# Performance work log

Hardware: AMD Instinct MI355X
Metric: run time of the kernel (lower is better)

## Reference

```python
import jax, jax.numpy as jnp
import numpy as np

B, D, C = 1024, 512, 100000
S, M = 64.0, 0.35
EPS = 1e-12  # torch F.normalize eps


def setup_inputs() -> dict:
    key = jax.random.key(0)
    k1, k2, k3 = jax.random.split(key, 3)
    inp = jax.random.normal(k1, (B, D), dtype=jnp.float32)
    label = jax.random.randint(k2, (B,), 0, C, dtype=jnp.int64)
    weight = jax.random.normal(k3, (C, D), dtype=jnp.float32) * (6.0 / (C + D)) ** 0.5
    return {"input": inp, "label": label, "weight": weight}


def _l2norm(x):
    n = jnp.linalg.norm(x, axis=-1, keepdims=True)
    return x / jnp.maximum(n, EPS)


def reference(input, label, weight):
    # cosine similarities: [B, C]
    cosine = _l2norm(input) @ _l2norm(weight).T
    # subtract margin only at the label position (no dense one-hot materialized)
    rows = jnp.arange(cosine.shape[0])
    logits = S * cosine.at[rows, label].add(-M)
    # cross-entropy (mean reduction)
    logz = jax.nn.logsumexp(logits, axis=-1)
    tgt = logits[rows, label]
    return jnp.mean(logz - tgt)
```

## Files before the change

kernel.cpp:

```cpp
#include <hip/hip_runtime.h>
#include <hip/hip_bf16.h>
#include <stdint.h>

#define NB 1024
#define ND 512
#define NC 100000
#define NCT 782
#define NCT2 391
#define SSCALE 64.0f
#define SMARG 22.4f

typedef __attribute__((ext_vector_type(8))) short bf16x8;
typedef __attribute__((ext_vector_type(4))) float f32x4;
typedef __attribute__((ext_vector_type(4))) int   i32x4;

__device__ __forceinline__ unsigned int f2bf(float f) {
    union { float f; unsigned int u; } c; c.f = f;
    return (c.u + 0x7fffu + ((c.u >> 16) & 1u)) >> 16;
}

__device__ __forceinline__ float wave_sum(float v) {
    #pragma unroll
    for (int m = 32; m > 0; m >>= 1) v += __shfl_xor(v, m);
    return v;
}

__device__ __forceinline__ float wave_max(float v) {
    #pragma unroll
    for (int m = 32; m > 0; m >>= 1) v = fmaxf(v, __shfl_xor(v, m));
    return v;
}

__device__ __forceinline__ void load_lds16(const void* g, void* l) {
    auto gp = reinterpret_cast<const __attribute__((address_space(1))) void*>(
        (uintptr_t)g);
    auto lp = reinterpret_cast<__attribute__((address_space(3))) void*>(
        (uint32_t)(uintptr_t)l);
    __builtin_amdgcn_global_load_lds(gp, lp, 16, 0, 0);
}

__global__ void norm_input_i8_k(const float* __restrict__ x,
                                unsigned char* __restrict__ xq,
                                float* __restrict__ isx) {
    int lane = threadIdx.x & 63;
    int row = blockIdx.x * 4 + (threadIdx.x >> 6);
    const float* xr = x + (size_t)row * ND + lane * 8;
    float4 v0 = ((const float4*)xr)[0];
    float4 v1 = ((const float4*)xr)[1];
    float ss = v0.x*v0.x + v0.y*v0.y + v0.z*v0.z + v0.w*v0.w
             + v1.x*v1.x + v1.y*v1.y + v1.z*v1.z + v1.w*v1.w;
    ss = wave_sum(ss);
    float inv = 1.0f / fmaxf(sqrtf(ss), 1e-12f);
    float f[8] = {v0.x*inv, v0.y*inv, v0.z*inv, v0.w*inv,
                  v1.x*inv, v1.y*inv, v1.z*inv, v1.w*inv};
    float ma = 0.0f;
    #pragma unroll
    for (int j = 0; j < 8; ++j) ma = fmaxf(ma, fabsf(f[j]));
    ma = wave_max(ma);
    ma = fmaxf(ma, 1e-12f);
    float s = 127.0f / ma;
    int q[8];
    #pragma unroll
    for (int j = 0; j < 8; ++j) q[j] = (int)rintf(f[j] * s);
    uint2 o;
    o.x = (q[0]&255) | ((q[1]&255)<<8) | ((q[2]&255)<<16) | ((unsigned)(q[3]&255)<<24);
    o.y = (q[4]&255) | ((q[5]&255)<<8) | ((q[6]&255)<<16) | ((unsigned)(q[7]&255)<<24);
    *(uint2*)(xq + (size_t)row * ND + lane * 8) = o;
    if (lane == 0) isx[row] = ma * (1.0f / 127.0f);
}

__global__ void conv_weight_i8_k(const float* __restrict__ w,
                                 unsigned char* __restrict__ wq,
                                 float* __restrict__ isw) {
    int lane = threadIdx.x & 63;
    int row = blockIdx.x * 4 + (threadIdx.x >> 6);
    const float* wr = w + (size_t)row * ND + lane * 8;
    float4 v0 = ((const float4*)wr)[0];
    float4 v1 = ((const float4*)wr)[1];
    float ss = v0.x*v0.x + v0.y*v0.y + v0.z*v0.z + v0.w*v0.w
             + v1.x*v1.x + v1.y*v1.y + v1.z*v1.z + v1.w*v1.w;
    ss = wave_sum(ss);
    float inv = 1.0f / fmaxf(sqrtf(ss), 1e-12f);
    float f[8] = {v0.x*inv, v0.y*inv, v0.z*inv, v0.w*inv,
                  v1.x*inv, v1.y*inv, v1.z*inv, v1.w*inv};
    float ma = 0.0f;
    #pragma unroll
    for (int j = 0; j < 8; ++j) ma = fmaxf(ma, fabsf(f[j]));
    ma = wave_max(ma);
    ma = fmaxf(ma, 1e-12f);
    float s = 127.0f / ma;
    int q[8];
    #pragma unroll
    for (int j = 0; j < 8; ++j) q[j] = (int)rintf(f[j] * s);
    uint2 o;
    o.x = (q[0]&255) | ((q[1]&255)<<8) | ((q[2]&255)<<16) | ((unsigned)(q[3]&255)<<24);
    o.y = (q[4]&255) | ((q[5]&255)<<8) | ((q[6]&255)<<16) | ((unsigned)(q[7]&255)<<24);
    *(uint2*)(wq + (size_t)row * ND + lane * 8) = o;
    if (lane == 0) isw[row] = ma * (1.0f / 127.0f);
}

__global__ __launch_bounds__(512, 2) void gemm_i8_k(
    const unsigned char* __restrict__ xq, const unsigned char* __restrict__ wq,
    const float* __restrict__ isx, const float* __restrict__ isw,
    const int* __restrict__ label,
    float* __restrict__ partial, float* __restrict__ tgt) {

    __shared__ __align__(16) char Tb[2][32768];
    __shared__ float rowsum[4][256];
    __shared__ int labs[256];
    __shared__ float isxs[256];
    __shared__ float isws[256];

    const int orig = blockIdx.x + (blockIdx.y << 2);
    const int xcd = orig & 7, idx = orig >> 3;
    const int wg = (xcd < 4 ? xcd * 196 : 784 + (xcd - 4) * 195) + idx;
    const int bx = wg & 3;
    const int by = wg >> 2;

    const int tid = threadIdx.x;
    const int lane = tid & 63;
    const int wid  = tid >> 6;
    const int brow0 = bx * 256;
    const int crow0 = by * 256;

    if (tid < 256) {
        labs[tid] = label[brow0 + tid];
        isxs[tid] = isx[brow0 + tid];
        int c = crow0 + tid;
        isws[tid] = (c < NC) ? isw[c] : 1.0f;
    }

    const unsigned char* gsrc[4];
    int ldst[4];
    #pragma unroll
    for (int i = 0; i < 4; ++i) {
        int cidx = wid * 256 + i * 64 + lane;
        int r = cidx >> 3, s = cidx & 7;
        int l = s ^ (r & 7);
        if (l < 4) {
            gsrc[i] = xq + (size_t)(brow0 + r) * ND + l * 16;
        } else {
            int wrow = crow0 + r;
            if (wrow >= NC) wrow = NC - 1;
            gsrc[i] = wq + (size_t)wrow * ND + (l - 4) * 16;
        }
        ldst[i] = cidx * 16;
    }

    const int wr = wid >> 2, wc = wid & 3;
    const int l15 = lane & 15, l4 = lane >> 4;

    i32x4 acc[8][4];
    #pragma unroll
    for (int i = 0; i < 8; ++i)
        #pragma unroll
        for (int j = 0; j < 4; ++j) acc[i][j] = (i32x4){0, 0, 0, 0};

    #pragma unroll
    for (int i = 0; i < 4; ++i) load_lds16(gsrc[i], &Tb[0][ldst[i]]);

    #pragma unroll
    for (int t = 0; t < 8; ++t) {
        __syncthreads();
        const char* cb = Tb[t & 1];
        i32x4 a0[4], a1[4], bfr[4];
        #pragma unroll
        for (int n = 0; n < 4; ++n) {
            int br = wc * 64 + n * 16 + l15;
            bfr[n] = *(const i32x4*)(cb + br * 128 + (((4 + l4) << 4) ^ ((br & 7) << 4)));
        }
        #pragma unroll
        for (int m = 0; m < 4; ++m) {
            int ar = wr * 128 + m * 16 + l15;
            a0[m] = *(const i32x4*)(cb + ar * 128 + ((l4 << 4) ^ ((ar & 7) << 4)));
        }
        if (t < 7) {
            char* nb = Tb[(t + 1) & 1];
            #pragma unroll
            for (int i = 0; i < 4; ++i)
                load_lds16(gsrc[i] + (t + 1) * 64, &nb[ldst[i]]);
        }
        #pragma unroll
        for (int m = 0; m < 4; ++m) {
            int ar = wr * 128 + (4 + m) * 16 + l15;
            a1[m] = *(const i32x4*)(cb + ar * 128 + ((l4 << 4) ^ ((ar & 7) << 4)));
        }
        __builtin_amdgcn_s_setprio(1);
        #pragma unroll
        for (int m = 0; m < 4; ++m)
            #pragma unroll
            for (int n = 0; n < 4; ++n)
                acc[m][n] = __builtin_amdgcn_mfma_i32_16x16x64_i8(
                    a0[m], bfr[n], acc[m][n], 0, 0, 0);
        __builtin_amdgcn_s_setprio(0);
        __builtin_amdgcn_s_setprio(1);
        #pragma unroll
        for (int m = 0; m < 4; ++m)
            #pragma unroll
            for (int n = 0; n < 4; ++n)
                acc[4 + m][n] = __builtin_amdgcn_mfma_i32_16x16x64_i8(
                    a1[m], bfr[n], acc[4 + m][n], 0, 0, 0);
        __builtin_amdgcn_s_setprio(0);
    }

    float rs[8][4];
    #pragma unroll
    for (int mi = 0; mi < 8; ++mi)
        #pragma unroll
        for (int r = 0; r < 4; ++r) rs[mi][r] = 0.0f;

    #pragma unroll
    for (int mi = 0; mi < 8; ++mi) {
        #pragma unroll
        for (int ni = 0; ni < 4; ++ni) {
            int ci = wc * 64 + ni * 16 + l15;
            int gc = crow0 + ci;
            float iw = isws[ci] * SSCALE;
            i32x4 av = acc[mi][ni];
            #pragma unroll
            for (int r = 0; r < 4; ++r) {
                int tr = wr * 128 + mi * 16 + l4 * 4 + r;
                float z = (float)av[r] * isxs[tr] * iw;
                if (gc == labs[tr]) {
                    z -= SMARG;
                    tgt[brow0 + tr] = z;
                }
                float e = (gc < NC) ? __expf(z - 64.0f) : 0.0f;
                rs[mi][r] += e;
            }
        }
    }
    #pragma unroll
    for (int mi = 0; mi < 8; ++mi)
        #pragma unroll
        for (int r = 0; r < 4; ++r) {
            float v = rs[mi][r];
            v += __shfl_xor(v, 1); v += __shfl_xor(v, 2);
            v += __shfl_xor(v, 4); v += __shfl_xor(v, 8);
            rs[mi][r] = v;
        }
    if (l15 == 0) {
        #pragma unroll
        for (int mi = 0; mi < 8; ++mi)
            #pragma unroll
            for (int r = 0; r < 4; ++r)
                rowsum[wc][wr * 128 + mi * 16 + l4 * 4 + r] = rs[mi][r];
    }
    __syncthreads();
    if (tid < 256)
        partial[(size_t)by * NB + brow0 + tid] =
            rowsum[0][tid] + rowsum[1][tid] + rowsum[2][tid] + rowsum[3][tid];
}

__global__ void norm_input_k(const float* __restrict__ x, unsigned short* __restrict__ xn) {
    int lane = threadIdx.x & 63;
    int row = blockIdx.x * 4 + (threadIdx.x >> 6);
    const float* xr = x + row * ND + lane * 8;
    float4 v0 = ((const float4*)xr)[0];
    float4 v1 = ((const float4*)xr)[1];
    float ss = v0.x*v0.x + v0.y*v0.y + v0.z*v0.z + v0.w*v0.w
             + v1.x*v1.x + v1.y*v1.y + v1.z*v1.z + v1.w*v1.w;
    ss = wave_sum(ss);
    float inv = 1.0f / fmaxf(sqrtf(ss), 1e-12f);
    int4 o;
    o.x = f2bf(v0.x*inv) | (f2bf(v0.y*inv) << 16);
    o.y = f2bf(v0.z*inv) | (f2bf(v0.w*inv) << 16);
    o.z = f2bf(v1.x*inv) | (f2bf(v1.y*inv) << 16);
    o.w = f2bf(v1.z*inv) | (f2bf(v1.w*inv) << 16);
    *(int4*)(xn + row * ND + lane * 8) = o;
}

__global__ void norm_weight_k(const float* __restrict__ w, float* __restrict__ invw) {
    int lane = threadIdx.x & 63;
    int row = blockIdx.x * 4 + (threadIdx.x >> 6);
    if (row >= NC) return;
    const float* wr = w + (size_t)row * ND + lane * 8;
    float4 v0 = ((const float4*)wr)[0];
    float4 v1 = ((const float4*)wr)[1];
    float ss = v0.x*v0.x + v0.y*v0.y + v0.z*v0.z + v0.w*v0.w
             + v1.x*v1.x + v1.y*v1.y + v1.z*v1.z + v1.w*v1.w;
    ss = wave_sum(ss);
    if (lane == 0) invw[row] = 1.0f / fmaxf(sqrtf(ss), 1e-12f);
}

__global__ __launch_bounds__(256) void gemm_fb_k(
    const unsigned short* __restrict__ xn, const float* __restrict__ w,
    const float* __restrict__ invw, const int* __restrict__ label,
    float* __restrict__ partial, float* __restrict__ tgt) {

    __shared__ __align__(16) char As[16384];
    __shared__ __align__(16) char Ws[16384];
    __shared__ float rowsum[2][128];
    __shared__ int labs[128];

    const int tid = threadIdx.x;
    const int brow0 = blockIdx.x * 128;
    const int crow0 = blockIdx.y * 128;

    if (tid < 128) labs[tid] = label[brow0 + tid];

    int arow[4], ac16[4];
    float wiv[4];
    bool  wval[4];
    #pragma unroll
    for (int i = 0; i < 4; ++i) {
        int idx = tid + i * 256;
        arow[i] = idx >> 3; ac16[i] = idx & 7;
        int grow = crow0 + (idx >> 3);
        wval[i] = grow < NC;
        wiv[i]  = wval[i] ? invw[grow] : 0.0f;
    }

    const int lane = tid & 63;
    const int wid  = tid >> 6;
    const int wr = wid >> 1, wc = wid & 1;
    const int l15 = lane & 15, l4 = lane >> 4;

    f32x4 acc[4][4];
    #pragma unroll
    for (int i = 0; i < 4; ++i)
        #pragma unroll
        for (int j = 0; j < 4; ++j) acc[i][j] = (f32x4){0.f, 0.f, 0.f, 0.f};

    for (int ks = 0; ks < 8; ++ks) {
        const int kbase = ks * 64;
        __syncthreads();
        #pragma unroll
        for (int i = 0; i < 4; ++i) {
            int row = arow[i], c16 = ac16[i];
            int4 v = *(const int4*)(xn + (brow0 + row) * ND + kbase + c16 * 8);
            *(int4*)(As + row * 128 + ((c16 * 16) ^ ((row & 7) << 4))) = v;
        }
        #pragma unroll
        for (int i = 0; i < 4; ++i) {
            int row = arow[i], c8 = ac16[i];
            float4 w0 = {0.f,0.f,0.f,0.f}, w1 = {0.f,0.f,0.f,0.f};
            if (wval[i]) {
                const float* wp = w + (size_t)(crow0 + row) * ND + kbase + c8 * 8;
                w0 = ((const float4*)wp)[0];
                w1 = ((const float4*)wp)[1];
            }
            float iv = wiv[i];
            int4 o;
            o.x = f2bf(w0.x*iv) | (f2bf(w0.y*iv) << 16);
            o.y = f2bf(w0.z*iv) | (f2bf(w0.w*iv) << 16);
            o.z = f2bf(w1.x*iv) | (f2bf(w1.y*iv) << 16);
            o.w = f2bf(w1.z*iv) | (f2bf(w1.w*iv) << 16);
            *(int4*)(Ws + row * 128 + ((c8 * 16) ^ ((row & 7) << 4))) = o;
        }
        __syncthreads();
        #pragma unroll
        for (int k32 = 0; k32 < 2; ++k32) {
            const int kb = k32 * 64 + l4 * 16;
            bf16x8 a[4], b[4];
            #pragma unroll
            for (int mi = 0; mi < 4; ++mi) {
                int ar = wr * 64 + mi * 16 + l15;
                a[mi] = *(const bf16x8*)(As + ar * 128 + (kb ^ ((ar & 7) << 4)));
            }
            #pragma unroll
            for (int ni = 0; ni < 4; ++ni) {
                int br = wc * 64 + ni * 16 + l15;
                b[ni] = *(const bf16x8*)(Ws + br * 128 + (kb ^ ((br & 7) << 4)));
            }
            #pragma unroll
            for (int mi = 0; mi < 4; ++mi)
                #pragma unroll
                for (int ni = 0; ni < 4; ++ni)
                    acc[mi][ni] = __builtin_amdgcn_mfma_f32_16x16x32_bf16(
                        a[mi], b[ni], acc[mi][ni], 0, 0, 0);
        }
    }

    float rs[4][4];
    #pragma unroll
    for (int mi = 0; mi < 4; ++mi)
        #pragma unroll
        for (int r = 0; r < 4; ++r) rs[mi][r] = 0.0f;

    #pragma unroll
    for (int mi = 0; mi < 4; ++mi) {
        #pragma unroll
        for (int ni = 0; ni < 4; ++ni) {
            int gc = crow0 + wc * 64 + ni * 16 + l15;
            f32x4 av = acc[mi][ni];
            #pragma unroll
            for (int r = 0; r < 4; ++r) {
                int tr = wr * 64 + mi * 16 + l4 * 4 + r;
                float z = SSCALE * av[r];
                if (gc == labs[tr]) {
                    z -= SMARG;
                    tgt[brow0 + tr] = z;
                }
                float e = (gc < NC) ? __expf(z - 64.0f) : 0.0f;
                rs[mi][r] += e;
            }
        }
    }
    #pragma unroll
    for (int mi = 0; mi < 4; ++mi)
        #pragma unroll
        for (int r = 0; r < 4; ++r) {
            float v = rs[mi][r];
            v += __shfl_xor(v, 1); v += __shfl_xor(v, 2);
            v += __shfl_xor(v, 4); v += __shfl_xor(v, 8);
            rs[mi][r] = v;
        }
    if (l15 == 0) {
        #pragma unroll
        for (int mi = 0; mi < 4; ++mi)
            #pragma unroll
            for (int r = 0; r < 4; ++r)
                rowsum[wc][wr * 64 + mi * 16 + l4 * 4 + r] = rs[mi][r];
    }
    __syncthreads();
    if (tid < 128)
        partial[(size_t)blockIdx.y * NB + brow0 + tid] = rowsum[0][tid] + rowsum[1][tid];
}

__global__ void row_lse_k(const float* __restrict__ partial, const float* __restrict__ tgt,
                          float* __restrict__ lossb, int nt) {
    int b = blockIdx.x;
    float s = 0.0f;
    for (int i = threadIdx.x; i < nt; i += 256)
        s += partial[(size_t)i * NB + b];
    s = wave_sum(s);
    __shared__ float wsum[4];
    if ((threadIdx.x & 63) == 0) wsum[threadIdx.x >> 6] = s;
    __syncthreads();
    if (threadIdx.x == 0)
        lossb[b] = 64.0f + logf(wsum[0] + wsum[1] + wsum[2] + wsum[3]) - tgt[b];
}

__global__ void mean_k(const float* __restrict__ lossb, float* __restrict__ out) {
    float s = 0.0f;
    for (int i = threadIdx.x; i < NB; i += 256) s += lossb[i];
    s = wave_sum(s);
    __shared__ float wsum[4];
    if ((threadIdx.x & 63) == 0) wsum[threadIdx.x >> 6] = s;
    __syncthreads();
    if (threadIdx.x == 0)
        out[0] = (wsum[0] + wsum[1] + wsum[2] + wsum[3]) * (1.0f / (float)NB);
}

extern "C" void kernel_launch(void* const* d_in, const int* in_sizes, int n_in,
                              void* d_out, int out_size, void* d_ws, size_t ws_size,
                              hipStream_t stream) {
    const float* x     = (const float*)d_in[0];
    const int*   label = (const int*)d_in[1];
    const float* w     = (const float*)d_in[2];
    float* out = (float*)d_out;
    char* ws = (char*)d_ws;

    const size_t WQ_B   = (size_t)NC * ND;
    const size_t ISW_B  = 400000;
    const size_t XQ_B   = (size_t)NB * ND;
    const size_t ISX_B  = 4096;
    const size_t PART2  = (size_t)NCT2 * NB * 4;
    const size_t FAST_REQ = WQ_B + ISW_B + XQ_B + ISX_B + PART2 + 8192;

    if (ws_size >= FAST_REQ) {
        unsigned char* wq      = (unsigned char*)(ws);
        float*         iswv    = (float*)(ws + WQ_B);
        unsigned char* xq      = (unsigned char*)(ws + WQ_B + ISW_B);
        float*         isxv    = (float*)(ws + WQ_B + ISW_B + XQ_B);
        float*         partial = (float*)(ws + WQ_B + ISW_B + XQ_B + ISX_B);
        float*         tgt     = (float*)(ws + WQ_B + ISW_B + XQ_B + ISX_B + PART2);
        float*         lossb   = (float*)(ws + WQ_B + ISW_B + XQ_B + ISX_B + PART2 + 4096);

        norm_input_i8_k <<<NB / 4, 256, 0, stream>>>(x, xq, isxv);
        conv_weight_i8_k<<<NC / 4, 256, 0, stream>>>(w, wq, iswv);
        dim3 grid(4, NCT2);
        gemm_i8_k<<<grid, 512, 0, stream>>>(xq, wq, isxv, iswv, label, partial, tgt);
        row_lse_k<<<NB, 256, 0, stream>>>(partial, tgt, lossb, NCT2);
        mean_k<<<1, 256, 0, stream>>>(lossb, out);
    } else {
        float*          invw    = (float*)(ws);
        unsigned short* xn      = (unsigned short*)(ws + 400384);
        float*          partial = (float*)(ws + 400384 + 1048576);
        float*          tgt     = (float*)(ws + 400384 + 1048576 + 3203072);
        float*          lossb   = (float*)(ws + 400384 + 1048576 + 3203072 + 4096);

        norm_input_k <<<NB / 4, 256, 0, stream>>>(x, xn);
        norm_weight_k<<<NC / 4, 256, 0, stream>>>(w, invw);
        dim3 grid(8, NCT);
        gemm_fb_k<<<grid, 256, 0, stream>>>(xn, w, invw, label, partial, tgt);
        row_lse_k<<<NB, 256, 0, stream>>>(partial, tgt, lossb, NCT);
        mean_k<<<1, 256, 0, stream>>>(lossb, out);
    }
}
```

Before: 164.0 us.

## Load weight fragments directly from global into registers, stage only input in LDS

The int8 GEMM now keeps only the input (A) tile in a smaller double-buffered LDS array, laid out so each lane reads its MFMA fragment contiguously. The weight (B) fragments are loaded straight from global memory into registers and prefetched one k-step ahead. This halves LDS traffic and LDS footprint, which may allow higher occupancy, and removes the swizzled LDS reads for B. In exchange each wave issues uncoalesced-ish 16-byte global loads for weights, depends on the register prefetch hiding latency, and uses more registers.

Result: slower. 207.5 us (+26.5%).

```diff
diff --git a/kernel.cpp b/kernel.cpp
--- a/kernel.cpp
+++ b/kernel.cpp
@@ -105,7 +105,7 @@
     const int* __restrict__ label,
     float* __restrict__ partial, float* __restrict__ tgt) {
 
-    __shared__ __align__(16) char Tb[2][32768];
+    __shared__ __align__(16) char Ab[2][16384];
     __shared__ float rowsum[4][256];
     __shared__ int labs[256];
     __shared__ float isxs[256];
@@ -130,77 +130,63 @@
         isws[tid] = (c < NC) ? isw[c] : 1.0f;
     }
 
-    const unsigned char* gsrc[4];
-    int ldst[4];
-    #pragma unroll
-    for (int i = 0; i < 4; ++i) {
-        int cidx = wid * 256 + i * 64 + lane;
-        int r = cidx >> 3, s = cidx & 7;
-        int l = s ^ (r & 7);
-        if (l < 4) {
-            gsrc[i] = xq + (size_t)(brow0 + r) * ND + l * 16;
-        } else {
-            int wrow = crow0 + r;
-            if (wrow >= NC) wrow = NC - 1;
-            gsrc[i] = wq + (size_t)wrow * ND + (l - 4) * 16;
-        }
-        ldst[i] = cidx * 16;
-    }
+    const int sr = tid & 255;
+    const int sc0 = tid >> 8;
+    const unsigned char* gA0 = xq + (size_t)(brow0 + sr) * ND + sc0 * 16;
+    const unsigned char* gA1 = gA0 + 32;
+    const int d0 = tid * 16;
+    const int d1 = d0 + 8192;
 
     const int wr = wid >> 2, wc = wid & 3;
     const int l15 = lane & 15, l4 = lane >> 4;
 
+    const unsigned char* gW[4];
+    #pragma unroll
+    for (int n = 0; n < 4; ++n) {
+        int br = crow0 + wc * 64 + n * 16 + l15;
+        if (br >= NC) br = NC - 1;
+        gW[n] = wq + (size_t)br * ND + l4 * 16;
+    }
+
     i32x4 acc[8][4];
     #pragma unroll
     for (int i = 0; i < 8; ++i)
         #pragma unroll
         for (int j = 0; j < 4; ++j) acc[i][j] = (i32x4){0, 0, 0, 0};
 
-    #pragma unroll
-    for (int i = 0; i < 4; ++i) load_lds16(gsrc[i], &Tb[0][ldst[i]]);
+    load_lds16(gA0, &Ab[0][d0]);
+    load_lds16(gA1, &Ab[0][d1]);
+    i32x4 wcur[4], wnxt[4];
+    #pragma unroll
+    for (int n = 0; n < 4; ++n) wcur[n] = *(const i32x4*)(gW[n]);
+    __syncthreads();
 
     #pragma unroll
     for (int t = 0; t < 8; ++t) {
-        __syncthreads();
-        const char* cb = Tb[t & 1];
-        i32x4 a0[4], a1[4], bfr[4];
-        #pragma unroll
-        for (int n = 0; n < 4; ++n) {
-            int br = wc * 64 + n * 16 + l15;
-            bfr[n] = *(const i32x4*)(cb + br * 128 + (((4 + l4) << 4) ^ ((br & 7) << 4)));
-        }
-        #pragma unroll
-        for (int m = 0; m < 4; ++m) {
-            int ar = wr * 128 + m * 16 + l15;
-            a0[m] = *(const i32x4*)(cb + ar * 128 + ((l4 << 4) ^ ((ar & 7) << 4)));
-        }
         if (t < 7) {
-            char* nb = Tb[(t + 1) & 1];
-            #pragma unroll
-            for (int i = 0; i < 4; ++i)
-                load_lds16(gsrc[i] + (t + 1) * 64, &nb[ldst[i]]);
-        }
-        #pragma unroll
-        for (int m = 0; m < 4; ++m) {
-            int ar = wr * 128 + (4 + m) * 16 + l15;
-            a1[m] = *(const i32x4*)(cb + ar * 128 + ((l4 << 4) ^ ((ar & 7) << 4)));
-        }
+            const int ko = (t + 1) * 64;
+            load_lds16(gA0 + ko, &Ab[(t + 1) & 1][d0]);
+            load_lds16(gA1 + ko, &Ab[(t + 1) & 1][d1]);
+            #pragma unroll
+            for (int n = 0; n < 4; ++n) wnxt[n] = *(const i32x4*)(gW[n] + ko);
+        }
+        const char* cb = Ab[t & 1];
+        const int abase = l4 * 4096 + (wr * 128 + l15) * 16;
+        i32x4 afr[8];
+        #pragma unroll
+        for (int m = 0; m < 8; ++m)
+            afr[m] = *(const i32x4*)(cb + abase + m * 256);
         __builtin_amdgcn_s_setprio(1);
         #pragma unroll
-        for (int m = 0; m < 4; ++m)
+        for (int m = 0; m < 8; ++m)
             #pragma unroll
             for (int n = 0; n < 4; ++n)
                 acc[m][n] = __builtin_amdgcn_mfma_i32_16x16x64_i8(
-                    a0[m], bfr[n], acc[m][n], 0, 0, 0);
+                    afr[m], wcur[n], acc[m][n], 0, 0, 0);
         __builtin_amdgcn_s_setprio(0);
-        __builtin_amdgcn_s_setprio(1);
-        #pragma unroll
-        for (int m = 0; m < 4; ++m)
-            #pragma unroll
-            for (int n = 0; n < 4; ++n)
-                acc[4 + m][n] = __builtin_amdgcn_mfma_i32_16x16x64_i8(
-                    a1[m], bfr[n], acc[4 + m][n], 0, 0, 0);
-        __builtin_amdgcn_s_setprio(0);
+        #pragma unroll
+        for (int n = 0; n < 4; ++n) wcur[n] = wnxt[n];
+        if (t < 7) __syncthreads();
     }
 
     float rs[8][4];
@@ -239,6 +225,7 @@
             v += __shfl_xor(v, 4); v += __shfl_xor(v, 8);
             rs[mi][r] = v;
         }
+    __syncthreads();
     if (l15 == 0) {
         #pragma unroll
         for (int mi = 0; mi < 8; ++mi)
```
